# Optimization experiments

Hardware: AMD Instinct MI355X
Metric: run time of the kernel (lower is better)

Reference implementation:

```python
import jax, jax.numpy as jnp
import numpy as np

RANGE0 = -3.0   # x/y offset of grid
VOX = 6.0       # voxel size -> nx = ny = 1
EPS_BN = 1e-3   # BatchNorm eps used in PFN / conv head
EPS_MLP = 1e-5  # default BN eps inside pyg-style MLP


def _bn_masked(h, w, gamma, beta, eps):
    # training-mode BatchNorm1d over valid rows only (w is [N,1] 0/1 mask)
    n = jnp.maximum(w.sum(), 1.0)
    m = (h * w).sum(0) / n
    v = (jnp.square(h - m) * w).sum(0) / n
    return (h - m) * jax.lax.rsqrt(v + eps) * gamma + beta


def _bn(h, gamma, beta, eps):
    # training-mode BatchNorm over axis 0 (spatial dims are 1x1)
    m = h.mean(0)
    v = jnp.square(h - m).mean(0)
    return (h - m) * jax.lax.rsqrt(v + eps) * gamma + beta


def _pillar_branch(x, batch, B, W1, g1, bb1, W2, g2, bb2):
    # dynamic voxelization: grid is 1x1, so pillar id == batch id for in-range points
    pts, extra = x[:, :3], x[:, 3:]
    cx = jnp.floor((pts[:, 0] - RANGE0) / VOX)
    cy = jnp.floor((pts[:, 1] - RANGE0) / VOX)
    valid = (cx >= 0) & (cx < 1) & (cy >= 0) & (cy < 1)
    seg = jnp.where(valid, batch, B).astype(jnp.int32)  # invalid -> dummy segment B
    w = valid.astype(x.dtype)[:, None]

    cnt = jax.ops.segment_sum(w[:, 0], seg, num_segments=B + 1)        # [B+1]
    psum = jax.ops.segment_sum(pts * w, seg, num_segments=B + 1)       # [B+1,3]
    pmean = psum / jnp.maximum(cnt, 1.0)[:, None]
    f_cluster = pts - pmean[seg]                                        # [N,3]
    f_center = jnp.stack([pts[:, 0] - (cx * VOX + RANGE0),
                          pts[:, 1] - (cy * VOX + RANGE0),
                          pts[:, 2]], axis=1)                           # [N,3]
    feat = jnp.concatenate([pts, f_cluster, f_center, extra], axis=1)  # [N,12]

    # PFN layer 1: Lin(12,32,no bias) + BN + ReLU + scatter_max + concat -> [N,64]
    h = feat @ W1
    h = jax.nn.relu(_bn_masked(h, w, g1, bb1, EPS_BN))
    hmax = jax.ops.segment_max(h, seg, num_segments=B + 1)
    hmax = jnp.where(jnp.isfinite(hmax), hmax, 0.0)
    h = jnp.concatenate([h, hmax[seg]], axis=1)                        # [N,64]

    # PFN layer 2 (last): Lin(64,64,no bias) + BN + ReLU + scatter_max -> [B,64]
    h = h @ W2
    h = jax.nn.relu(_bn_masked(h, w, g2, bb2, EPS_BN))
    pmax = jax.ops.segment_max(h, seg, num_segments=B + 1)[:B]
    pmax = jnp.where((cnt[:B] > 0)[:, None],
                     jnp.where(jnp.isfinite(pmax), pmax, 0.0), 0.0)
    return pmax  # BEV features, grid is 1x1 so scatter_to_bev == identity


def setup_inputs() -> dict:
    key = jax.random.key(0)
    ks = jax.random.split(key, 10)
    N, B = 500000, 64
    x = jax.random.normal(ks[0], (N, 6), jnp.float32)
    x2 = jax.random.normal(ks[1], (N, 6), jnp.float32)
    batch = jnp.sort(jax.random.randint(ks[2], (N,), 0, B)).astype(jnp.int32)
    batch2 = jnp.sort(jax.random.randint(ks[3], (N,), 0, B)).astype(jnp.int32)
    y = jax.random.randint(ks[4], (B,), 0, 5).astype(jnp.int32)

    def w(k, shape, fan_in):
        return (jax.random.normal(k, shape, jnp.float32) / np.sqrt(fan_in)).astype(jnp.float32)

    return dict(
        x=x, x2=x2, batch=batch, batch2=batch2, y=y,
        W1=w(ks[5], (12, 32), 12), g1=jnp.ones(32, jnp.float32), bb1=jnp.zeros(32, jnp.float32),
        W2=w(ks[6], (64, 64), 64), g2=jnp.ones(64, jnp.float32), bb2=jnp.zeros(64, jnp.float32),
        Wc=w(ks[7], (1024, 64), 64), gc=jnp.ones(1024, jnp.float32), bc=jnp.zeros(1024, jnp.float32),
        Wm1=w(ks[8], (1024, 64), 1024), bm1=jnp.zeros(64, jnp.float32),
        gm=jnp.ones(64, jnp.float32), bm=jnp.zeros(64, jnp.float32),
        Wm2=w(ks[9], (64, 5), 64), bm2=jnp.zeros(5, jnp.float32),
    )


def reference(x, x2, batch, batch2, y,
              W1, g1, bb1, W2, g2, bb2,
              Wc, gc, bc, Wm1, bm1, gm, bm, Wm2, bm2):
    B = y.shape[0]
    p1 = _pillar_branch(x, batch, B, W1, g1, bb1, W2, g2, bb2)    # [B,64]
    p2 = _pillar_branch(x2, batch2, B, W1, g1, bb1, W2, g2, bb2)  # [B,64]
    # conv_2d: 1x1 conv 64->1024 on 1x1 BEV == linear, + BN2d + ReLU
    z1 = jax.nn.relu(_bn(p1 @ Wc.T, gc, bc, EPS_BN))              # [B,1024]
    z2 = jax.nn.relu(_bn(p2 @ Wc.T, gc, bc, EPS_BN))
    d = z2 - z1
    # MLP([1024,64]) = Lin + ReLU + BN, then Lin(64,5)
    h = _bn(jax.nn.relu(d @ Wm1 + bm1), gm, bm, EPS_MLP)
    logits = h @ Wm2 + bm2
    return jax.nn.log_softmax(logits, axis=-1)
```

## Files before the change

kernel.cpp:

```cpp
#include <hip/hip_runtime.h>
#include <float.h>
#include <math.h>

#define S0 16
#define SB 16

#define O_BOUNDS 0
#define O_W2BF   160
#define BR_BASE  1184
#define O_CNT    0
#define O_BIASP  64
#define O_UP     2112
#define O_P0PART 2304
#define O_SEGSR  30976
#define O_SEGZMX 33024
#define O_SEGSQ  35072
#define O_SEGMMX 39168
#define O_PMAX   43264
#define BRSZ     47360
#define O_D      (BR_BASE + 2*BRSZ)
#define O_HMLP   (O_D + 65536)

typedef __attribute__((ext_vector_type(8))) short short8;
typedef __attribute__((ext_vector_type(4))) float f32x4;

__device__ __forceinline__ int lower_bound_i(const int* a, int n, int v) {
    int lo = 0, hi = n;
    while (lo < hi) { int mid = (lo + hi) >> 1; if (a[mid] < v) lo = mid + 1; else hi = mid; }
    return lo;
}
__device__ __forceinline__ void atomicMaxF(float* a, float v) {
    if (v >= 0.f) atomicMax((int*)a, __float_as_int(v));
    else atomicMin((unsigned int*)a, (unsigned int)__float_as_int(v));
}
__device__ __forceinline__ bool is_valid(float p0, float p1) {
    return (floorf((p0 + 3.f) / 6.f) == 0.f) && (floorf((p1 + 3.f) / 6.f) == 0.f);
}
__device__ __forceinline__ unsigned short f2bf(float x) {
    unsigned int u = __float_as_uint(x);
    return (unsigned short)((u + 0x7FFFu + ((u >> 16) & 1u)) >> 16);
}

__global__ __launch_bounds__(256) void segBoundsKernel(const int* __restrict__ bt0, const int* __restrict__ bt1,
                                                       int N, float* ws) {
    int br = blockIdx.y;
    const int* batch = br ? bt1 : bt0;
    float* base = ws + BR_BASE + (size_t)br * BRSZ;
    int* bounds = (int*)(ws + O_BOUNDS) + br * 65;
    int t = threadIdx.x;
    if (t <= 64) bounds[t] = lower_bound_i(batch, N, t);
    #pragma unroll
    for (int r = 0; r < 8; r++) {
        int idx = t + r * 256;
        base[O_SEGSR + idx] = 0.f;
        base[O_SEGZMX + idx] = -FLT_MAX;
    }
    #pragma unroll
    for (int r = 0; r < 16; r++) {
        int idx = t + r * 256;
        base[O_SEGSQ + idx] = 0.f;
        base[O_SEGMMX + idx] = -FLT_MAX;
    }
}

__global__ __launch_bounds__(256) void pass0Kernel(const float* __restrict__ x0,
                                                   const float* __restrict__ x1,
                                                   int N, float* ws) {
    int br = blockIdx.y;
    const float* x = br ? x1 : x0;
    float* base = ws + BR_BASE + (size_t)br * BRSZ;
    const int* bounds = (const int*)(ws + O_BOUNDS) + br * 65;
    int b = blockIdx.x / S0, s = blockIdx.x % S0;
    int lo = bounds[b], hi = bounds[b + 1];
    int chunk = (hi - lo + S0 - 1) / S0;
    int beg = lo + s * chunk, end = min(hi, beg + chunk);

    float acc[28];
    #pragma unroll
    for (int k = 0; k < 28; k++) acc[k] = 0.f;

    for (int i = beg + (int)threadIdx.x; i < end; i += 256) {
        const float2* px = (const float2*)(x + (size_t)i * 6);
        float2 q0 = px[0], q1 = px[1], q2 = px[2];
        float f[6] = {q0.x, q0.y, q1.x, q1.y, q2.x, q2.y};
        if (is_valid(f[0], f[1])) {
            acc[0] += 1.f;
            #pragma unroll
            for (int k = 0; k < 6; k++) acc[1 + k] += f[k];
            int k = 7;
            #pragma unroll
            for (int a = 0; a < 6; a++)
                #pragma unroll
                for (int c = a; c < 6; c++) { acc[k] = fmaf(f[a], f[c], acc[k]); k++; }
        }
    }
    __shared__ float red[4][28];
    int w = threadIdx.x >> 6, l = threadIdx.x & 63;
    #pragma unroll
    for (int k = 0; k < 28; k++) {
        float v = acc[k];
        v += __shfl_xor(v, 1); v += __shfl_xor(v, 2); v += __shfl_xor(v, 4);
        v += __shfl_xor(v, 8); v += __shfl_xor(v, 16); v += __shfl_xor(v, 32);
        acc[k] = v;
    }
    if (l == 0) { for (int k = 0; k < 28; k++) red[w][k] = acc[k]; }
    __syncthreads();
    if (threadIdx.x < 28) {
        float v = red[0][threadIdx.x] + red[1][threadIdx.x] + red[2][threadIdx.x] + red[3][threadIdx.x];
        base[O_P0PART + (size_t)(b * S0 + s) * 28 + threadIdx.x] = v;
    }
}

__global__ __launch_bounds__(256) void bn1CoefKernel(const float* __restrict__ W1,
                                                     const float* __restrict__ W2,
                                                     const float* __restrict__ g1,
                                                     const float* __restrict__ bb1, float* ws) {
    int br = blockIdx.y;
    float* base = ws + BR_BASE + (size_t)br * BRSZ;
    int t = threadIdx.x;
    __shared__ float SEG[64][28];
    __shared__ float Ul[6][32];
    __shared__ float BIASS[64][32];
    __shared__ float aS[32], abS[32];
    __shared__ float red[8][32], red2[8][32];

    if (t < 192) {
        int k = t / 32, c = t & 31;
        Ul[k][c] = (k < 3) ? (W1[k*32+c] + W1[(k+3)*32+c] + W1[(k+6)*32+c]) : W1[(k+6)*32+c];
    }
    #pragma unroll
    for (int r = 0; r < 4; r++) {
        int idx = t + r * 256;
        unsigned int lo = f2bf(W2[2*idx]), hi = f2bf(W2[2*idx + 1]);
        ((unsigned int*)(ws + O_W2BF))[idx] = lo | (hi << 16);
    }
    #pragma unroll
    for (int r = 0; r < 7; r++) {
        int idx = t + r * 256;
        int b = idx / 28, k = idx % 28;
        float v = 0.f;
        for (int sc = 0; sc < S0; sc++) v += base[O_P0PART + (size_t)(b*S0+sc)*28 + k];
        SEG[b][k] = v;
    }
    __syncthreads();
    if (t < 64) base[O_CNT + t] = SEG[t][0];

    int c = t & 31, bg = t >> 5;
    float c32 = 3.f * (W1[6*32+c] + W1[7*32+c]);
    float ps1 = 0.f, pss = 0.f;
    for (int j = 0; j < 8; j++) {
        int b = bg * 8 + j;
        float cnt = SEG[b][0];
        float cn = fmaxf(cnt, 1.f);
        float bias = c32 - (SEG[b][1]/cn)*W1[3*32+c] - (SEG[b][2]/cn)*W1[4*32+c] - (SEG[b][3]/cn)*W1[5*32+c];
        BIASS[b][c] = bias;
        float dotv = 0.f;
        #pragma unroll
        for (int i = 0; i < 6; i++) dotv = fmaf(SEG[b][1+i], Ul[i][c], dotv);
        float quad = 0.f;
        int k = 7;
        #pragma unroll
        for (int i = 0; i < 6; i++) {
            quad = fmaf(SEG[b][k], Ul[i][c] * Ul[i][c], quad); k++;
            #pragma unroll
            for (int j2 = i + 1; j2 < 6; j2++) { quad = fmaf(SEG[b][k], 2.f * Ul[i][c] * Ul[j2][c], quad); k++; }
        }
        ps1 += dotv + cnt * bias;
        pss += quad + 2.f * bias * dotv + cnt * bias * bias;
    }
    red[bg][c] = ps1; red2[bg][c] = pss;
    __syncthreads();
    if (bg == 0) {
        float s1 = 0.f, sq = 0.f;
        for (int k = 0; k < 8; k++) { s1 += red[k][c]; sq += red2[k][c]; }
        float tot = 0.f;
        for (int k = 0; k < 64; k++) tot += SEG[k][0];
        float n = fmaxf(tot, 1.f);
        float m = s1 / n, v = sq / n - m * m;
        float a = g1[c] * rsqrtf(v + 0.001f);
        aS[c] = a; abS[c] = bb1[c] - m * a;
    }
    __syncthreads();
    if (t < 192) {
        int cc = t & 31;
        base[O_UP + t] = aS[cc] * Ul[t / 32][cc];
    }
    #pragma unroll
    for (int r = 0; r < 8; r++) {
        int idx = t + r * 256;
        int cc = idx & 31;
        base[O_BIASP + idx] = fmaf(aS[cc], BIASS[idx >> 5][cc], abS[cc]);
    }
}

__global__ __launch_bounds__(256) void passBKernel(const float* __restrict__ x0,
                                                   const float* __restrict__ x1,
                                                   int N, float* ws) {
    int br = blockIdx.y;
    const float* x = br ? x1 : x0;
    float* base = ws + BR_BASE + (size_t)br * BRSZ;
    const int* bounds = (const int*)(ws + O_BOUNDS) + br * 65;
    int b = blockIdx.x / SB, s = blockIdx.x % SB;
    int lo = bounds[b], hi = bounds[b + 1];
    int chunk = (hi - lo + SB - 1) / SB;
    int beg = lo + s * chunk, end = min(hi, beg + chunk);
    int npts = end - beg;
    int ntiles = npts > 0 ? ((npts + 63) >> 6) : 0;
    int ntiles2 = (ntiles + 1) & ~1;

    int t = threadIdx.x;
    int w = t >> 6, l = t & 63, n0 = l & 15, g4 = l >> 4;
    int myoff = 16 * w + n0;
    int c8 = 8 * g4;

    const unsigned short* w2u = (const unsigned short*)(ws + O_W2BF);
    short8 bfrag[4];
    #pragma unroll
    for (int ct = 0; ct < 4; ct++)
        #pragma unroll
        for (int j = 0; j < 8; j++)
            bfrag[ct][j] = (short)w2u[(c8 + j) * 64 + 16 * ct + n0];

    float uj[8][6], biasp[8];
    #pragma unroll
    for (int j = 0; j < 8; j++) {
        #pragma unroll
        for (int k = 0; k < 6; k++) uj[j][k] = base[O_UP + k * 32 + c8 + j];
        biasp[j] = base[O_BIASP + b * 32 + c8 + j];
    }

    float srelu[8], zmx[8];
    #pragma unroll
    for (int j = 0; j < 8; j++) { srelu[j] = 0.f; zmx[j] = -FLT_MAX; }
    f32x4 sq[4], mxa[4];
    #pragma unroll
    for (int ct = 0; ct < 4; ct++) {
        sq[ct] = (f32x4){0, 0, 0, 0};
        mxa[ct] = (f32x4){-FLT_MAX, -FLT_MAX, -FLT_MAX, -FLT_MAX};
    }

    float2 xa0, xa1, xa2, xb0, xb1, xb2;
#define LOADP(d0, d1, d2, tk) do { \
        int idxc_ = beg + (tk) * 64 + myoff; \
        int idxl_ = max(min(idxc_, end - 1), 0); \
        const float2* px_ = (const float2*)(x + (size_t)idxl_ * 6); \
        d0 = px_[0]; d1 = px_[1]; d2 = px_[2]; } while (0)

#define PROCESS(q0, q1, q2, tk) do { \
        float p0 = q0.x, p1 = q0.y, p2 = q1.x, e0 = q1.y, e1 = q2.x, e2 = q2.y; \
        bool val = (beg + (tk) * 64 + myoff < end) && is_valid(p0, p1); \
        float r8[8]; \
        _Pragma("unroll") \
        for (int j = 0; j < 8; j++) { \
            float z = fmaf(p0, uj[j][0], fmaf(p1, uj[j][1], fmaf(p2, uj[j][2], \
                      fmaf(e0, uj[j][3], fmaf(e1, uj[j][4], fmaf(e2, uj[j][5], biasp[j])))))); \
            float zsel = val ? z : -FLT_MAX; \
            zmx[j] = fmaxf(zmx[j], zsel); \
            float r = fmaxf(zsel, 0.f); \
            srelu[j] += r; \
            r8[j] = r; \
        } \
        unsigned int pk0, pk1, pk2, pk3; \
        asm("v_cvt_pk_bf16_f32 %0, %1, %2" : "=v"(pk0) : "v"(r8[0]), "v"(r8[1])); \
        asm("v_cvt_pk_bf16_f32 %0, %1, %2" : "=v"(pk1) : "v"(r8[2]), "v"(r8[3])); \
        asm("v_cvt_pk_bf16_f32 %0, %1, %2" : "=v"(pk2) : "v"(r8[4]), "v"(r8[5])); \
        asm("v_cvt_pk_bf16_f32 %0, %1, %2" : "=v"(pk3) : "v"(r8[6]), "v"(r8[7])); \
        uint4 pkv; pkv.x = pk0; pkv.y = pk1; pkv.z = pk2; pkv.w = pk3; \
        short8 af = __builtin_bit_cast(short8, pkv); \
        unsigned int bal32 = (unsigned int)__ballot(val); \
        float vmask[4]; \
        _Pragma("unroll") \
        for (int r = 0; r < 4; r++) \
            vmask[r] = ((bal32 >> (4 * g4 + r)) & 1u) ? 0.f : -FLT_MAX; \
        _Pragma("unroll") \
        for (int ct = 0; ct < 4; ct++) { \
            f32x4 cz = (f32x4){0, 0, 0, 0}; \
            f32x4 v = __builtin_amdgcn_mfma_f32_16x16x32_bf16(af, bfrag[ct], cz, 0, 0, 0); \
            _Pragma("unroll") \
            for (int r = 0; r < 4; r++) { \
                sq[ct][r] = fmaf(v[r], v[r], sq[ct][r]); \
                mxa[ct][r] = fmaxf(mxa[ct][r], v[r] + vmask[r]); \
            } \
        } } while (0)

    if (ntiles2 > 0) {
        LOADP(xa0, xa1, xa2, 0);
        LOADP(xb0, xb1, xb2, 1);
        for (int k = 0; k < ntiles2; k += 2) {
            float2 c0 = xa0, c1 = xa1, c2 = xa2;
            LOADP(xa0, xa1, xa2, k + 2);
            PROCESS(c0, c1, c2, k);
            float2 d0 = xb0, d1 = xb1, d2 = xb2;
            LOADP(xb0, xb1, xb2, k + 3);
            PROCESS(d0, d1, d2, k + 1);
        }
    }
#undef LOADP
#undef PROCESS

    __shared__ float redA[4][32], redB[4][32], redC[4][64], redD[4][64];
    float sred[8], zred[8];
    #pragma unroll
    for (int j = 0; j < 8; j++) {
        float sv = srelu[j], zv = zmx[j];
        sv += __shfl_xor(sv, 1); sv += __shfl_xor(sv, 2); sv += __shfl_xor(sv, 4); sv += __shfl_xor(sv, 8);
        zv = fmaxf(zv, __shfl_xor(zv, 1)); zv = fmaxf(zv, __shfl_xor(zv, 2));
        zv = fmaxf(zv, __shfl_xor(zv, 4)); zv = fmaxf(zv, __shfl_xor(zv, 8));
        sred[j] = sv; zred[j] = zv;
    }
    if (n0 == 0) {
        #pragma unroll
        for (int j = 0; j < 8; j++) { redA[w][c8 + j] = sred[j]; redB[w][c8 + j] = zred[j]; }
    }
    float sqs[4], mxs[4];
    #pragma unroll
    for (int ct = 0; ct < 4; ct++) {
        float sv = sq[ct][0] + sq[ct][1] + sq[ct][2] + sq[ct][3];
        float mv = fmaxf(fmaxf(mxa[ct][0], mxa[ct][1]), fmaxf(mxa[ct][2], mxa[ct][3]));
        sv += __shfl_xor(sv, 16); sv += __shfl_xor(sv, 32);
        mv = fmaxf(mv, __shfl_xor(mv, 16)); mv = fmaxf(mv, __shfl_xor(mv, 32));
        sqs[ct] = sv; mxs[ct] = mv;
    }
    if (l < 16) {
        #pragma unroll
        for (int ct = 0; ct < 4; ct++) { redC[w][16 * ct + l] = sqs[ct]; redD[w][16 * ct + l] = mxs[ct]; }
    }
    __syncthreads();
    if (t < 32) {
        atomicAdd(&base[O_SEGSR + b * 32 + t], redA[0][t] + redA[1][t] + redA[2][t] + redA[3][t]);
    } else if (t < 64) {
        int c = t - 32;
        float v = fmaxf(fmaxf(redB[0][c], redB[1][c]), fmaxf(redB[2][c], redB[3][c]));
        atomicMaxF(&base[O_SEGZMX + b * 32 + c], v);
    } else if (t < 128) {
        int c = t - 64;
        atomicAdd(&base[O_SEGSQ + b * 64 + c], redC[0][c] + redC[1][c] + redC[2][c] + redC[3][c]);
    } else if (t < 192) {
        int c = t - 128;
        float v = fmaxf(fmaxf(redD[0][c], redD[1][c]), fmaxf(redD[2][c], redD[3][c]));
        atomicMaxF(&base[O_SEGMMX + b * 64 + c], v);
    }
}

__global__ __launch_bounds__(256) void segFuseKernel(const float* __restrict__ W2,
                                                     const float* __restrict__ g2,
                                                     const float* __restrict__ bb2, float* ws) {
    int br = blockIdx.y;
    float* base = ws + BR_BASE + (size_t)br * BRSZ;
    int t = threadIdx.x;
    __shared__ float HM[64][32], SR[64][32];
    __shared__ float W2a[32][64], W2b[32][64];
    __shared__ float HS[64][64];
    __shared__ float CNTl[64];
    __shared__ float redS[4][64], redQ[4][64];
    __shared__ float AB2[2][64];

    #pragma unroll
    for (int r = 0; r < 8; r++) {
        int idx = t + r * 256;
        ((float*)W2a)[idx] = W2[idx];
        ((float*)W2b)[idx] = W2[2048 + idx];
    }
    if (t < 64) CNTl[t] = base[O_CNT + t];
    #pragma unroll
    for (int r = 0; r < 8; r++) {
        int idx = t + r * 256;
        int b = idx >> 5, c = idx & 31;
        SR[b][c] = base[O_SEGSR + idx];
        HM[b][c] = fmaxf(base[O_SEGZMX + idx], 0.f);
    }
    __syncthreads();
    int col = t & 63, bgq = t >> 6;
    float S = 0.f, Q = 0.f;
    for (int j = 0; j < 16; j++) {
        int b = bgq * 16 + j;
        float hs = 0.f, smm = 0.f;
        #pragma unroll
        for (int ch = 0; ch < 32; ch++) {
            hs  = fmaf(HM[b][ch], W2b[ch][col], hs);
            smm = fmaf(SR[b][ch], W2a[ch][col], smm);
        }
        HS[b][col] = hs;
        float cnt = CNTl[b];
        float qb = base[O_SEGSQ + b * 64 + col];
        S += smm + cnt * hs;
        Q += qb + 2.f * hs * smm + cnt * hs * hs;
    }
    redS[bgq][col] = S; redQ[bgq][col] = Q;
    __syncthreads();
    if (t < 64) {
        float Sv = redS[0][t] + redS[1][t] + redS[2][t] + redS[3][t];
        float Qv = redQ[0][t] + redQ[1][t] + redQ[2][t] + redQ[3][t];
        float tot = 0.f;
        for (int k = 0; k < 64; k++) tot += CNTl[k];
        float n = fmaxf(tot, 1.f);
        float m = Sv / n, v = Qv / n - m * m;
        float a = g2[t] * rsqrtf(v + 0.001f);
        AB2[0][t] = a; AB2[1][t] = bb2[t] - m * a;
    }
    __syncthreads();
    #pragma unroll
    for (int r = 0; r < 16; r++) {
        int idx = t + r * 256;
        int b = idx >> 6, c2 = idx & 63;
        float mv = base[O_SEGMMX + b * 64 + c2];
        float out = 0.f;
        if (CNTl[b] > 0.f) out = fmaxf(fmaf(AB2[0][c2], mv + HS[b][c2], AB2[1][c2]), 0.f);
        base[O_PMAX + b * 64 + c2] = out;
    }
}

__global__ __launch_bounds__(256) void dKernel(const float* __restrict__ Wc, const float* __restrict__ gc,
                                               const float* __restrict__ bc, float* ws) {
    __shared__ float P1s[64 * 65], P2s[64 * 65], WcS[4][64];
    int t = threadIdx.x;
    const float* p1 = ws + BR_BASE + O_PMAX;
    const float* p2 = ws + BR_BASE + BRSZ + O_PMAX;
    #pragma unroll
    for (int r = 0; r < 16; r++) {
        int idx = t + r * 256;
        int i2 = idx >> 6, c2 = idx & 63;
        P1s[i2 * 65 + c2] = p1[idx];
        P2s[i2 * 65 + c2] = p2[idx];
    }
    int jl = t >> 6, i = t & 63;
    int j = blockIdx.x * 4 + jl;
    WcS[jl][i] = Wc[(size_t)j * 64 + i];
    __syncthreads();
    float t1 = 0.f, t2 = 0.f;
    #pragma unroll
    for (int c = 0; c < 64; c++) {
        float wv = WcS[jl][c];
        t1 = fmaf(P1s[i * 65 + c], wv, t1);
        t2 = fmaf(P2s[i * 65 + c], wv, t2);
    }
    float m1 = t1, m2 = t2;
    for (int off = 32; off; off >>= 1) { m1 += __shfl_xor(m1, off); m2 += __shfl_xor(m2, off); }
    m1 *= (1.f / 64.f); m2 *= (1.f / 64.f);
    float d1 = t1 - m1, d2 = t2 - m2;
    float v1 = d1 * d1, v2 = d2 * d2;
    for (int off = 32; off; off >>= 1) { v1 += __shfl_xor(v1, off); v2 += __shfl_xor(v2, off); }
    v1 *= (1.f / 64.f); v2 *= (1.f / 64.f);
    float z1 = fmaxf(d1 * rsqrtf(v1 + 0.001f) * gc[j] + bc[j], 0.f);
    float z2 = fmaxf(d2 * rsqrtf(v2 + 0.001f) * gc[j] + bc[j], 0.f);
    ws[O_D + (size_t)j * 64 + i] = z2 - z1;
}

__global__ __launch_bounds__(256) void hKernel(const float* __restrict__ Wm1, const float* __restrict__ bm1,
                                               const float* __restrict__ gm, const float* __restrict__ bm,
                                               float* ws) {
    int cidx = blockIdx.x;
    int t = threadIdx.x;
    int i = t & 63, q = t >> 6;
    const float* dT = ws + O_D;
    float part = 0.f;
    for (int k = q * 256; k < q * 256 + 256; k++)
        part = fmaf(dT[(size_t)k * 64 + i], Wm1[(size_t)k * 64 + cidx], part);
    __shared__ float red[4][64];
    red[q][i] = part; __syncthreads();
    if (t < 64) {
        float u = red[0][t] + red[1][t] + red[2][t] + red[3][t] + bm1[cidx];
        u = fmaxf(u, 0.f);
        float m = u;
        for (int off = 32; off; off >>= 1) m += __shfl_xor(m, off);
        m *= (1.f / 64.f);
        float du = u - m;
        float v = du * du;
        for (int off = 32; off; off >>= 1) v += __shfl_xor(v, off);
        v *= (1.f / 64.f);
        ws[O_HMLP + (size_t)t * 64 + cidx] = du * rsqrtf(v + 1e-5f) * gm[cidx] + bm[cidx];
    }
}

__global__ void outKernel(const float* __restrict__ Wm2, const float* __restrict__ bm2,
                          const float* __restrict__ ws, float* out) {
    __shared__ float lg[64][5];
    __shared__ float lse[64];
    int t = threadIdx.x;
    {
        int i = t / 5, j = t % 5;
        const float* h = ws + O_HMLP;
        float acc = bm2[j];
        for (int k = 0; k < 64; k++) acc = fmaf(h[i * 64 + k], Wm2[k * 5 + j], acc);
        lg[i][j] = acc;
    }
    __syncthreads();
    if (t < 64) {
        float mxv = lg[t][0];
        for (int j = 1; j < 5; j++) mxv = fmaxf(mxv, lg[t][j]);
        float sv = 0.f;
        for (int j = 0; j < 5; j++) sv += expf(lg[t][j] - mxv);
        lse[t] = mxv + logf(sv);
    }
    __syncthreads();
    out[t] = lg[t / 5][t % 5] - lse[t / 5];
}

extern "C" void kernel_launch(void* const* d_in, const int* in_sizes, int n_in,
                              void* d_out, int out_size, void* d_ws, size_t ws_size,
                              hipStream_t stream) {
    const float* x0  = (const float*)d_in[0];
    const float* x1  = (const float*)d_in[1];
    const int*   bt0 = (const int*)d_in[2];
    const int*   bt1 = (const int*)d_in[3];
    const float* W1  = (const float*)d_in[5];
    const float* g1  = (const float*)d_in[6];
    const float* bb1 = (const float*)d_in[7];
    const float* W2  = (const float*)d_in[8];
    const float* g2  = (const float*)d_in[9];
    const float* bb2 = (const float*)d_in[10];
    const float* Wc  = (const float*)d_in[11];
    const float* gc  = (const float*)d_in[12];
    const float* bc  = (const float*)d_in[13];
    const float* Wm1 = (const float*)d_in[14];
    const float* bm1 = (const float*)d_in[15];
    const float* gm  = (const float*)d_in[16];
    const float* bm  = (const float*)d_in[17];
    const float* Wm2 = (const float*)d_in[18];
    const float* bm2 = (const float*)d_in[19];
    float* ws  = (float*)d_ws;
    float* out = (float*)d_out;
    int N = in_sizes[0] / 6;

    segBoundsKernel<<<dim3(1, 2),      dim3(256), 0, stream>>>(bt0, bt1, N, ws);
    pass0Kernel    <<<dim3(64*S0, 2),  dim3(256), 0, stream>>>(x0, x1, N, ws);
    bn1CoefKernel  <<<dim3(1, 2),      dim3(256), 0, stream>>>(W1, W2, g1, bb1, ws);
    passBKernel    <<<dim3(64*SB, 2),  dim3(256), 0, stream>>>(x0, x1, N, ws);
    segFuseKernel  <<<dim3(1, 2),      dim3(256), 0, stream>>>(W2, g2, bb2, ws);
    dKernel        <<<dim3(256),       dim3(256), 0, stream>>>(Wc, gc, bc, ws);
    hKernel        <<<dim3(64),        dim3(256), 0, stream>>>(Wm1, bm1, gm, bm, ws);
    outKernel      <<<dim3(1),         dim3(320), 0, stream>>>(Wm2, bm2, ws, out);
}
```

Baseline: 96.38 us.

## Parallelize segment bounds, prefetch point loads, reduce splits, drop max masking

Segment bounds are now computed by a grid-wide scan for batch-id transitions instead of per-thread binary search in a single block. pass0 gains a register prefetch of the next point, and passB moves from double to triple buffering of point loads. Split factors shrink (fewer blocks per segment, smaller partial workspace). Max tracking now works on post-ReLU values initialized to zero, which removes the ballot and mask work. The cost is longer serial loops per block, and the scan writes bounds for every segment, including empty ones, in a different way than before.

```diff
diff --git a/kernel.cpp b/kernel.cpp
--- a/kernel.cpp
+++ b/kernel.cpp
@@ -2,8 +2,8 @@
 #include <float.h>
 #include <math.h>
 
-#define S0 16
-#define SB 16
+#define S0 4
+#define SB 8
 
 #define O_BOUNDS 0
 #define O_W2BF   160
@@ -12,23 +12,18 @@
 #define O_BIASP  64
 #define O_UP     2112
 #define O_P0PART 2304
-#define O_SEGSR  30976
-#define O_SEGZMX 33024
-#define O_SEGSQ  35072
-#define O_SEGMMX 39168
-#define O_PMAX   43264
-#define BRSZ     47360
+#define O_SEGSR  9472
+#define O_SEGZMX 11520
+#define O_SEGSQ  13568
+#define O_SEGMMX 17664
+#define O_PMAX   21760
+#define BRSZ     25856
 #define O_D      (BR_BASE + 2*BRSZ)
 #define O_HMLP   (O_D + 65536)
 
 typedef __attribute__((ext_vector_type(8))) short short8;
 typedef __attribute__((ext_vector_type(4))) float f32x4;
 
-__device__ __forceinline__ int lower_bound_i(const int* a, int n, int v) {
-    int lo = 0, hi = n;
-    while (lo < hi) { int mid = (lo + hi) >> 1; if (a[mid] < v) lo = mid + 1; else hi = mid; }
-    return lo;
-}
 __device__ __forceinline__ void atomicMaxF(float* a, float v) {
     if (v >= 0.f) atomicMax((int*)a, __float_as_int(v));
     else atomicMin((unsigned int*)a, (unsigned int)__float_as_int(v));
@@ -47,19 +42,28 @@
     const int* batch = br ? bt1 : bt0;
     float* base = ws + BR_BASE + (size_t)br * BRSZ;
     int* bounds = (int*)(ws + O_BOUNDS) + br * 65;
-    int t = threadIdx.x;
-    if (t <= 64) bounds[t] = lower_bound_i(batch, N, t);
-    #pragma unroll
-    for (int r = 0; r < 8; r++) {
-        int idx = t + r * 256;
-        base[O_SEGSR + idx] = 0.f;
-        base[O_SEGZMX + idx] = -FLT_MAX;
-    }
-    #pragma unroll
-    for (int r = 0; r < 16; r++) {
-        int idx = t + r * 256;
-        base[O_SEGSQ + idx] = 0.f;
-        base[O_SEGMMX + idx] = -FLT_MAX;
+    int gid = blockIdx.x * 256 + threadIdx.x;
+    int stride = gridDim.x * 256;
+    for (int i = gid; i < N; i += stride) {
+        int b = batch[i];
+        int prev = (i == 0) ? -1 : batch[i - 1];
+        for (int v = prev + 1; v <= b; v++) bounds[v] = i;
+        if (i == N - 1) for (int v = b + 1; v <= 64; v++) bounds[v] = N;
+    }
+    if (blockIdx.x == 0) {
+        int t = threadIdx.x;
+        #pragma unroll
+        for (int r = 0; r < 8; r++) {
+            int idx = t + r * 256;
+            base[O_SEGSR + idx] = 0.f;
+            base[O_SEGZMX + idx] = 0.f;
+        }
+        #pragma unroll
+        for (int r = 0; r < 16; r++) {
+            int idx = t + r * 256;
+            base[O_SEGSQ + idx] = 0.f;
+            base[O_SEGMMX + idx] = 0.f;
+        }
     }
 }
 
@@ -79,10 +83,19 @@
     #pragma unroll
     for (int k = 0; k < 28; k++) acc[k] = 0.f;
 
-    for (int i = beg + (int)threadIdx.x; i < end; i += 256) {
-        const float2* px = (const float2*)(x + (size_t)i * 6);
-        float2 q0 = px[0], q1 = px[1], q2 = px[2];
-        float f[6] = {q0.x, q0.y, q1.x, q1.y, q2.x, q2.y};
+    int i0 = beg + (int)threadIdx.x;
+    float2 a0, a1, a2;
+    {
+        int ip = max(min(i0, end - 1), 0);
+        const float2* pp = (const float2*)(x + (size_t)ip * 6);
+        a0 = pp[0]; a1 = pp[1]; a2 = pp[2];
+    }
+    for (int i = i0; i < end; i += 256) {
+        float2 c0 = a0, c1 = a1, c2 = a2;
+        int ipn = max(min(i + 256, end - 1), 0);
+        const float2* pp = (const float2*)(x + (size_t)ipn * 6);
+        a0 = pp[0]; a1 = pp[1]; a2 = pp[2];
+        float f[6] = {c0.x, c0.y, c1.x, c1.y, c2.x, c2.y};
         if (is_valid(f[0], f[1])) {
             acc[0] += 1.f;
             #pragma unroll
@@ -206,7 +219,7 @@
     int beg = lo + s * chunk, end = min(hi, beg + chunk);
     int npts = end - beg;
     int ntiles = npts > 0 ? ((npts + 63) >> 6) : 0;
-    int ntiles2 = (ntiles + 1) & ~1;
+    int ntiles3 = ((ntiles + 2) / 3) * 3;
 
     int t = threadIdx.x;
     int w = t >> 6, l = t & 63, n0 = l & 15, g4 = l >> 4;
@@ -229,17 +242,17 @@
         biasp[j] = base[O_BIASP + b * 32 + c8 + j];
     }
 
-    float srelu[8], zmx[8];
-    #pragma unroll
-    for (int j = 0; j < 8; j++) { srelu[j] = 0.f; zmx[j] = -FLT_MAX; }
+    float srelu[8], rmx[8];
+    #pragma unroll
+    for (int j = 0; j < 8; j++) { srelu[j] = 0.f; rmx[j] = 0.f; }
     f32x4 sq[4], mxa[4];
     #pragma unroll
     for (int ct = 0; ct < 4; ct++) {
         sq[ct] = (f32x4){0, 0, 0, 0};
-        mxa[ct] = (f32x4){-FLT_MAX, -FLT_MAX, -FLT_MAX, -FLT_MAX};
-    }
-
-    float2 xa0, xa1, xa2, xb0, xb1, xb2;
+        mxa[ct] = (f32x4){0, 0, 0, 0};
+    }
+
+    float2 xa0, xa1, xa2, xb0, xb1, xb2, xc0, xc1, xc2;
 #define LOADP(d0, d1, d2, tk) do { \
         int idxc_ = beg + (tk) * 64 + myoff; \
         int idxl_ = max(min(idxc_, end - 1), 0); \
@@ -254,10 +267,10 @@
         for (int j = 0; j < 8; j++) { \
             float z = fmaf(p0, uj[j][0], fmaf(p1, uj[j][1], fmaf(p2, uj[j][2], \
                       fmaf(e0, uj[j][3], fmaf(e1, uj[j][4], fmaf(e2, uj[j][5], biasp[j])))))); \
-            float zsel = val ? z : -FLT_MAX; \
-            zmx[j] = fmaxf(zmx[j], zsel); \
-            float r = fmaxf(zsel, 0.f); \
+            float r = fmaxf(z, 0.f); \
+            r = val ? r : 0.f; \
             srelu[j] += r; \
+            rmx[j] = fmaxf(rmx[j], r); \
             r8[j] = r; \
         } \
         unsigned int pk0, pk1, pk2, pk3; \
@@ -267,11 +280,6 @@
         asm("v_cvt_pk_bf16_f32 %0, %1, %2" : "=v"(pk3) : "v"(r8[6]), "v"(r8[7])); \
         uint4 pkv; pkv.x = pk0; pkv.y = pk1; pkv.z = pk2; pkv.w = pk3; \
         short8 af = __builtin_bit_cast(short8, pkv); \
-        unsigned int bal32 = (unsigned int)__ballot(val); \
-        float vmask[4]; \
-        _Pragma("unroll") \
-        for (int r = 0; r < 4; r++) \
-            vmask[r] = ((bal32 >> (4 * g4 + r)) & 1u) ? 0.f : -FLT_MAX; \
         _Pragma("unroll") \
         for (int ct = 0; ct < 4; ct++) { \
             f32x4 cz = (f32x4){0, 0, 0, 0}; \
@@ -279,20 +287,24 @@
             _Pragma("unroll") \
             for (int r = 0; r < 4; r++) { \
                 sq[ct][r] = fmaf(v[r], v[r], sq[ct][r]); \
-                mxa[ct][r] = fmaxf(mxa[ct][r], v[r] + vmask[r]); \
+                mxa[ct][r] = fmaxf(mxa[ct][r], v[r]); \
             } \
         } } while (0)
 
-    if (ntiles2 > 0) {
+    if (ntiles3 > 0) {
         LOADP(xa0, xa1, xa2, 0);
         LOADP(xb0, xb1, xb2, 1);
-        for (int k = 0; k < ntiles2; k += 2) {
-            float2 c0 = xa0, c1 = xa1, c2 = xa2;
-            LOADP(xa0, xa1, xa2, k + 2);
-            PROCESS(c0, c1, c2, k);
-            float2 d0 = xb0, d1 = xb1, d2 = xb2;
-            LOADP(xb0, xb1, xb2, k + 3);
-            PROCESS(d0, d1, d2, k + 1);
+        LOADP(xc0, xc1, xc2, 2);
+        for (int k = 0; k < ntiles3; k += 3) {
+            float2 ta0 = xa0, ta1 = xa1, ta2 = xa2;
+            LOADP(xa0, xa1, xa2, k + 3);
+            PROCESS(ta0, ta1, ta2, k);
+            float2 tb0 = xb0, tb1 = xb1, tb2 = xb2;
+            LOADP(xb0, xb1, xb2, k + 4);
+            PROCESS(tb0, tb1, tb2, k + 1);
+            float2 tc0 = xc0, tc1 = xc1, tc2 = xc2;
+            LOADP(xc0, xc1, xc2, k + 5);
+            PROCESS(tc0, tc1, tc2, k + 2);
         }
     }
 #undef LOADP
@@ -302,7 +314,7 @@
     float sred[8], zred[8];
     #pragma unroll
     for (int j = 0; j < 8; j++) {
-        float sv = srelu[j], zv = zmx[j];
+        float sv = srelu[j], zv = rmx[j];
         sv += __shfl_xor(sv, 1); sv += __shfl_xor(sv, 2); sv += __shfl_xor(sv, 4); sv += __shfl_xor(sv, 8);
         zv = fmaxf(zv, __shfl_xor(zv, 1)); zv = fmaxf(zv, __shfl_xor(zv, 2));
         zv = fmaxf(zv, __shfl_xor(zv, 4)); zv = fmaxf(zv, __shfl_xor(zv, 8));
@@ -367,7 +379,7 @@
         int idx = t + r * 256;
         int b = idx >> 5, c = idx & 31;
         SR[b][c] = base[O_SEGSR + idx];
-        HM[b][c] = fmaxf(base[O_SEGZMX + idx], 0.f);
+        HM[b][c] = base[O_SEGZMX + idx];
     }
     __syncthreads();
     int col = t & 63, bgq = t >> 6;
@@ -522,7 +534,7 @@
     float* out = (float*)d_out;
     int N = in_sizes[0] / 6;
 
-    segBoundsKernel<<<dim3(1, 2),      dim3(256), 0, stream>>>(bt0, bt1, N, ws);
+    segBoundsKernel<<<dim3(128, 2),    dim3(256), 0, stream>>>(bt0, bt1, N, ws);
     pass0Kernel    <<<dim3(64*S0, 2),  dim3(256), 0, stream>>>(x0, x1, N, ws);
     bn1CoefKernel  <<<dim3(1, 2),      dim3(256), 0, stream>>>(W1, W2, g1, bb1, ws);
     passBKernel    <<<dim3(64*SB, 2),  dim3(256), 0, stream>>>(x0, x1, N, ws);
```

After: 86.42 us (median of 2 runs). 10.3% less time.
